# Kernel tuning notes

Measured on AMD Instinct MI355X. Metric: run time of the kernel, lower is better.

## Reference

```python
import jax, jax.numpy as jnp
import numpy as np

TEMPERATURE = 0.1
THRESHOLD = 0.2
EPS = 1e-12


def setup_inputs() -> dict:
    key = jax.random.key(0)
    k0, k1 = jax.random.split(key)
    f0 = jax.random.normal(k0, (1, 256, 80, 80), dtype=jnp.float32)
    f1 = jax.random.normal(k1, (1, 256, 80, 80), dtype=jnp.float32)
    return {"f0": f0, "f1": f1}


def reference(f0, f1):
    B, C, H0, W0 = f0.shape
    _, _, H1, W1 = f1.shape
    N0, N1 = H0 * W0, H1 * W1

    # (B, N, C), L2-normalized along C (matches F.normalize with eps clamp)
    f0_flat = f0.reshape(B, C, N0).transpose(0, 2, 1)
    f1_flat = f1.reshape(B, C, N1).transpose(0, 2, 1)
    f0n = f0_flat / jnp.maximum(jnp.linalg.norm(f0_flat, axis=-1, keepdims=True), EPS)
    f1n = f1_flat / jnp.maximum(jnp.linalg.norm(f1_flat, axis=-1, keepdims=True), EPS)

    # cosine similarity / temperature: (B, N0, N1)
    S = jnp.einsum('bnc,bmc->bnm', f0n, f1n) / TEMPERATURE
    # dual softmax
    P = jax.nn.softmax(S, axis=-1) * jax.nn.softmax(S, axis=-2)

    # mutual nearest-neighbor matching (B == 1 branch)
    conf = jnp.max(P[0], axis=-1)              # (N0,)
    indices0 = jnp.argmax(P[0], axis=-1)       # (N0,) row argmax
    indices1 = jnp.argmax(P[0], axis=-2)       # (N1,) column argmax
    ar0 = jnp.arange(N0)
    mutual = indices1[indices0] == ar0
    valid = mutual & (conf > THRESHOLD)        # (N0,) bool

    # fixed-shape (jit-friendly) match outputs: full grid, zeroed where invalid
    mkpts0 = jnp.stack([ar0 % W0, ar0 // W0], axis=1).astype(jnp.float32)
    mkpts1 = jnp.stack([indices0 % W1, indices0 // W1], axis=1).astype(jnp.float32)
    vf = valid[:, None].astype(jnp.float32)
    mkpts0 = mkpts0 * vf
    mkpts1 = mkpts1 * vf
    mconf = jnp.where(valid, conf, 0.0)

    return (P, mkpts0, mkpts1, mconf, valid)
```

## Files before the change

### kernel.cpp

```cpp
#include <hip/hip_runtime.h>

#define N0 6400
#define NC 256
#define WW 80

using half8   = __attribute__((ext_vector_type(8))) _Float16;
using floatx4 = __attribute__((ext_vector_type(4))) float;
#define GLOBAL_AS __attribute__((address_space(1)))
#define LDS_AS    __attribute__((address_space(3)))

__device__ __forceinline__ unsigned long long packvi(float v, int i) {
    return ((unsigned long long)__float_as_uint(v) << 32) | (unsigned int)i;
}

__global__ __launch_bounds__(256) void knorm(const float* __restrict__ f0,
                                             const float* __restrict__ f1,
                                             float* __restrict__ inv0,
                                             float* __restrict__ inv1) {
    int t = blockIdx.x * 256 + threadIdx.x;
    const float* src = (t < N0) ? f0 : f1;
    int n = (t < N0) ? t : (t - N0);
    float s = 0.f;
#pragma unroll 8
    for (int c = 0; c < NC; ++c) {
        float v = src[c * N0 + n];
        s += v * v;
    }
    float inv = 1.0f / fmaxf(sqrtf(s), 1e-12f);
    if (t < N0) inv0[n] = inv; else inv1[n] = inv;
}

__global__ __launch_bounds__(256) void ktrans(const float* __restrict__ f0,
                                              const float* __restrict__ f1,
                                              const float* __restrict__ inv0,
                                              const float* __restrict__ inv1,
                                              _Float16* __restrict__ A2,
                                              _Float16* __restrict__ B2) {
    __shared__ float tile[32][33];
    const float* src = blockIdx.z ? f1 : f0;
    const float* inv = blockIdx.z ? inv1 : inv0;
    _Float16* dst    = blockIdx.z ? B2 : A2;
    int t = threadIdx.x;
    int n0 = blockIdx.x * 32, c0 = blockIdx.y * 32;
    int tx = t & 31, ty = t >> 5;
#pragma unroll
    for (int u = 0; u < 4; ++u)
        tile[ty + u * 8][tx] = src[(c0 + ty + u * 8) * N0 + n0 + tx];
    __syncthreads();
    int row = t >> 3;
    int cg  = (t & 7) * 4;
    int n = n0 + row;
    float iv = inv[n];
    union { ushort4 u4; _Float16 h[4]; } pk;
#pragma unroll
    for (int u = 0; u < 4; ++u)
        pk.h[u] = (_Float16)(tile[cg + u][row] * iv);
    *(ushort4*)&dst[n * NC + c0 + cg] = pk.u4;
}

__device__ __forceinline__ void stage_panel(const _Float16* __restrict__ G,
                                            unsigned short* lds, int r0, int tid) {
    int rl = tid >> 3;
    int ch = ((tid & 7) ^ (rl & 7)) * 8;
#pragma unroll
    for (int kk = 0; kk < 4; ++kk)
#pragma unroll
        for (int g = 0; g < 4; ++g) {
            const _Float16* ga = G + (r0 + g * 32 + rl) * NC + kk * 64 + ch;
            __builtin_amdgcn_global_load_lds((const GLOBAL_AS unsigned int*)ga,
                (LDS_AS unsigned int*)&lds[kk * 8192 + g * 2048 + tid * 8], 16, 0, 0);
        }
}

__device__ __forceinline__ void tile_mfma(const unsigned short* ldsA,
                                          const unsigned short* ldsB,
                                          int lane, int wm, int wn,
                                          floatx4 acc[4][4]) {
    int q = lane >> 4;
#pragma unroll
    for (int s = 0; s < 8; ++s) {
        int c  = s * 4 + q;
        int kk = c >> 3, cq = c & 7;
        half8 af[4], bf[4];
#pragma unroll
        for (int mt = 0; mt < 4; ++mt) {
            int ra = wm * 64 + mt * 16 + (lane & 15);
            af[mt] = *(const half8*)&ldsA[kk * 8192 + ra * 64 + ((cq ^ (ra & 7)) * 8)];
            int rb = wn * 64 + mt * 16 + (lane & 15);
            bf[mt] = *(const half8*)&ldsB[kk * 8192 + rb * 64 + ((cq ^ (rb & 7)) * 8)];
        }
#pragma unroll
        for (int mt = 0; mt < 4; ++mt)
#pragma unroll
            for (int nt = 0; nt < 4; ++nt)
                acc[mt][nt] = __builtin_amdgcn_mfma_f32_16x16x32_f16(
                    af[mt], bf[nt], acc[mt][nt], 0, 0, 0);
    }
}

__global__ __launch_bounds__(256, 1) void kgemm1(const _Float16* __restrict__ A2,
                                                 const _Float16* __restrict__ B2,
                                                 float* __restrict__ rowsum,
                                                 float* __restrict__ colsum) {
    __shared__ __align__(16) unsigned short ldsA[32768], ldsB[32768];
    int tid = threadIdx.x, lane = tid & 63, wave = tid >> 6;
    int wm = wave & 1, wn = wave >> 1, q = lane >> 4;
    int i0 = blockIdx.x * 128, jp = blockIdx.y * 1280;

    stage_panel(A2, ldsA, i0, tid);
    float rsum[4][4] = {};

    for (int jt = 0; jt < 10; ++jt) {
        __syncthreads();
        stage_panel(B2, ldsB, jp + jt * 128, tid);
        __syncthreads();
        floatx4 acc[4][4] = {};
        tile_mfma(ldsA, ldsB, lane, wm, wn, acc);

        float csum[4] = {0.f, 0.f, 0.f, 0.f};
#pragma unroll
        for (int mt = 0; mt < 4; ++mt)
#pragma unroll
            for (int r = 0; r < 4; ++r) {
                float rv = 0.f;
#pragma unroll
                for (int nt = 0; nt < 4; ++nt) {
                    float e = __expf(10.0f * acc[mt][nt][r]);
                    rv += e; csum[nt] += e;
                }
                rsum[mt][r] += rv;
            }
#pragma unroll
        for (int nt = 0; nt < 4; ++nt) {
            csum[nt] += __shfl_xor(csum[nt], 16);
            csum[nt] += __shfl_xor(csum[nt], 32);
        }
        if (lane < 16)
#pragma unroll
            for (int nt = 0; nt < 4; ++nt)
                atomicAdd(&colsum[jp + jt * 128 + wn * 64 + nt * 16 + lane], csum[nt]);
    }
#pragma unroll
    for (int mt = 0; mt < 4; ++mt)
#pragma unroll
        for (int r = 0; r < 4; ++r) {
            float v = rsum[mt][r];
            v += __shfl_xor(v, 1);
            v += __shfl_xor(v, 2);
            v += __shfl_xor(v, 4);
            v += __shfl_xor(v, 8);
            if ((lane & 15) == 0)
                atomicAdd(&rowsum[i0 + wm * 64 + mt * 16 + q * 4 + r], v);
        }
}

__global__ __launch_bounds__(256, 1) void kgemm2(const _Float16* __restrict__ A2,
                                                 const _Float16* __restrict__ B2,
                                                 const float* __restrict__ rowsum,
                                                 const float* __restrict__ colsum,
                                                 float* __restrict__ P,
                                                 unsigned long long* __restrict__ rowbest,
                                                 unsigned long long* __restrict__ colbest) {
    __shared__ __align__(16) unsigned short ldsA[32768], ldsB[32768];
    int tid = threadIdx.x, lane = tid & 63, wave = tid >> 6;
    int wm = wave & 1, wn = wave >> 1, q = lane >> 4;
    int i0 = blockIdx.x * 128, jp = blockIdx.y * 1280;

    stage_panel(A2, ldsA, i0, tid);

    float ir[4][4];
#pragma unroll
    for (int mt = 0; mt < 4; ++mt) {
        float4 v4 = *(const float4*)&rowsum[i0 + wm * 64 + mt * 16 + q * 4];
        ir[mt][0] = 1.0f / v4.x; ir[mt][1] = 1.0f / v4.y;
        ir[mt][2] = 1.0f / v4.z; ir[mt][3] = 1.0f / v4.w;
    }

    unsigned long long rbv[4][4] = {};

    for (int jt = 0; jt < 10; ++jt) {
        __syncthreads();
        stage_panel(B2, ldsB, jp + jt * 128, tid);
        __syncthreads();
        floatx4 acc[4][4] = {};
        tile_mfma(ldsA, ldsB, lane, wm, wn, acc);

        int cb0 = jp + jt * 128 + wn * 64 + (lane & 15);
        float ic[4];
#pragma unroll
        for (int nt = 0; nt < 4; ++nt) ic[nt] = 1.0f / colsum[cb0 + nt * 16];

        unsigned long long colb[4] = {0ull, 0ull, 0ull, 0ull};
#pragma unroll
        for (int mt = 0; mt < 4; ++mt) {
            int rb0 = i0 + wm * 64 + mt * 16 + q * 4;
#pragma unroll
            for (int r = 0; r < 4; ++r) {
                int row = rb0 + r;
#pragma unroll
                for (int nt = 0; nt < 4; ++nt) {
                    float pv = __expf(20.0f * acc[mt][nt][r]) * ir[mt][r] * ic[nt];
                    P[row * N0 + cb0 + nt * 16] = pv;
                    unsigned long long pr = packvi(pv, cb0 + nt * 16);
                    if (pr > rbv[mt][r]) rbv[mt][r] = pr;
                    unsigned long long pc = packvi(pv, row);
                    if (pc > colb[nt]) colb[nt] = pc;
                }
            }
        }
#pragma unroll
        for (int nt = 0; nt < 4; ++nt) {
            unsigned long long o = __shfl_xor(colb[nt], 16);
            if (o > colb[nt]) colb[nt] = o;
            o = __shfl_xor(colb[nt], 32);
            if (o > colb[nt]) colb[nt] = o;
        }
        if (lane < 16)
#pragma unroll
            for (int nt = 0; nt < 4; ++nt)
                atomicMax(&colbest[cb0 + nt * 16], colb[nt]);
    }
#pragma unroll
    for (int mt = 0; mt < 4; ++mt)
#pragma unroll
        for (int r = 0; r < 4; ++r) {
            unsigned long long v = rbv[mt][r];
#pragma unroll
            for (int s = 1; s < 16; s <<= 1) {
                unsigned long long o = __shfl_xor(v, s);
                if (o > v) v = o;
            }
            if ((lane & 15) == 0)
                atomicMax(&rowbest[i0 + wm * 64 + mt * 16 + q * 4 + r], v);
        }
}

__global__ __launch_bounds__(256) void kmatch(const unsigned long long* __restrict__ rowbest,
                                              const unsigned long long* __restrict__ colbest,
                                              float* __restrict__ out) {
    int i = blockIdx.x * 256 + threadIdx.x;
    unsigned long long rb = rowbest[i];
    float conf = __uint_as_float((unsigned int)(rb >> 32));
    int jj = (int)(rb & 0xffffffffu);
    unsigned long long cb = colbest[jj];
    int i2 = (int)(cb & 0xffffffffu);
    bool valid = (i2 == i) && (conf > 0.2f);
    float vf = valid ? 1.0f : 0.0f;

    float* mk0   = out + 40960000;
    float* mk1   = out + 40972800;
    float* mconf = out + 40985600;
    float* vout  = out + 40992000;
    mk0[i * 2 + 0] = vf * (float)(i % WW);
    mk0[i * 2 + 1] = vf * (float)(i / WW);
    mk1[i * 2 + 0] = vf * (float)(jj % WW);
    mk1[i * 2 + 1] = vf * (float)(jj / WW);
    mconf[i] = valid ? conf : 0.0f;
    vout[i]  = vf;
}

extern "C" void kernel_launch(void* const* d_in, const int* in_sizes, int n_in,
                              void* d_out, int out_size, void* d_ws, size_t ws_size,
                              hipStream_t stream) {
    const float* f0 = (const float*)d_in[0];
    const float* f1 = (const float*)d_in[1];
    float* out = (float*)d_out;

    _Float16* A2 = (_Float16*)d_ws;
    _Float16* B2 = A2 + 6400 * 256;
    float* inv0   = (float*)(B2 + 6400 * 256);
    float* inv1   = inv0 + 6400;
    float* rowsum = inv1 + 6400;
    float* colsum = rowsum + 6400;
    unsigned long long* rowbest = (unsigned long long*)(colsum + 6400);
    unsigned long long* colbest = rowbest + 6400;

    hipMemsetAsync(rowsum, 0, 153600, stream);

    knorm<<<50, 256, 0, stream>>>(f0, f1, inv0, inv1);
    ktrans<<<dim3(200, 8, 2), 256, 0, stream>>>(f0, f1, inv0, inv1, A2, B2);
    kgemm1<<<dim3(50, 5), 256, 0, stream>>>(A2, B2, rowsum, colsum);
    kgemm2<<<dim3(50, 5), 256, 0, stream>>>(A2, B2, rowsum, colsum,
                                            out, rowbest, colbest);
    kmatch<<<25, 256, 0, stream>>>(rowbest, colbest, out);
}
```

Measured before the change: 275.1 us.

## Restructure GEMM kernels with register-resident A, double-buffered B, partial-buffer reductions

The GEMM kernels now use 512 threads with the A panel held in registers, and they double-buffer the B panel in LDS so the next tile loads while the current one computes. Row and column sums and argmax values are written to per-block partial buffers and combined by separate reduce kernels, replacing global atomics and the memset. Argmax comparisons use the log-domain score instead of the exponentiated P, and P is written with vectorized nontemporal stores. The norm kernel is split across two channel halves for more parallelism. Costs are two extra launches and larger workspace traffic. The log-domain argmax risks tie-breaking differences from the reference.

```diff
diff --git a/kernel.cpp b/kernel.cpp
--- a/kernel.cpp
+++ b/kernel.cpp
@@ -15,30 +15,29 @@
 
 __global__ __launch_bounds__(256) void knorm(const float* __restrict__ f0,
                                              const float* __restrict__ f1,
-                                             float* __restrict__ inv0,
-                                             float* __restrict__ inv1) {
-    int t = blockIdx.x * 256 + threadIdx.x;
-    const float* src = (t < N0) ? f0 : f1;
-    int n = (t < N0) ? t : (t - N0);
+                                             float* __restrict__ snorm) {
+    int g = blockIdx.x * 256 + threadIdx.x;
+    int h = (g >= 12800) ? 1 : 0;
+    int j = g - h * 12800;
+    const float* src = (j < N0) ? f0 : f1;
+    int n = (j < N0) ? j : (j - N0);
+    int c0 = h * 128;
     float s = 0.f;
 #pragma unroll 8
-    for (int c = 0; c < NC; ++c) {
-        float v = src[c * N0 + n];
+    for (int c = 0; c < 128; ++c) {
+        float v = src[(c0 + c) * N0 + n];
         s += v * v;
     }
-    float inv = 1.0f / fmaxf(sqrtf(s), 1e-12f);
-    if (t < N0) inv0[n] = inv; else inv1[n] = inv;
+    snorm[g] = s;
 }
 
 __global__ __launch_bounds__(256) void ktrans(const float* __restrict__ f0,
                                               const float* __restrict__ f1,
-                                              const float* __restrict__ inv0,
-                                              const float* __restrict__ inv1,
+                                              const float* __restrict__ snorm,
                                               _Float16* __restrict__ A2,
                                               _Float16* __restrict__ B2) {
     __shared__ float tile[32][33];
     const float* src = blockIdx.z ? f1 : f0;
-    const float* inv = blockIdx.z ? inv1 : inv0;
     _Float16* dst    = blockIdx.z ? B2 : A2;
     int t = threadIdx.x;
     int n0 = blockIdx.x * 32, c0 = blockIdx.y * 32;
@@ -50,7 +49,9 @@
     int row = t >> 3;
     int cg  = (t & 7) * 4;
     int n = n0 + row;
-    float iv = inv[n];
+    int j = (blockIdx.z ? N0 : 0) + n;
+    float s = snorm[j] + snorm[12800 + j];
+    float iv = 1.0f / fmaxf(sqrtf(s), 1e-12f);
     union { ushort4 u4; _Float16 h[4]; } pk;
 #pragma unroll
     for (int u = 0; u < 4; ++u)
@@ -58,192 +59,259 @@
     *(ushort4*)&dst[n * NC + c0 + cg] = pk.u4;
 }
 
-__device__ __forceinline__ void stage_panel(const _Float16* __restrict__ G,
-                                            unsigned short* lds, int r0, int tid) {
+__device__ __forceinline__ void stage_full(const _Float16* __restrict__ G,
+                                           unsigned short* lds, int r0, int tid) {
     int rl = tid >> 3;
     int ch = ((tid & 7) ^ (rl & 7)) * 8;
 #pragma unroll
     for (int kk = 0; kk < 4; ++kk)
 #pragma unroll
-        for (int g = 0; g < 4; ++g) {
-            const _Float16* ga = G + (r0 + g * 32 + rl) * NC + kk * 64 + ch;
+        for (int g = 0; g < 2; ++g) {
+            const _Float16* ga = G + (r0 + g * 64 + rl) * NC + kk * 64 + ch;
             __builtin_amdgcn_global_load_lds((const GLOBAL_AS unsigned int*)ga,
-                (LDS_AS unsigned int*)&lds[kk * 8192 + g * 2048 + tid * 8], 16, 0, 0);
-        }
-}
-
-__device__ __forceinline__ void tile_mfma(const unsigned short* ldsA,
-                                          const unsigned short* ldsB,
-                                          int lane, int wm, int wn,
-                                          floatx4 acc[4][4]) {
+                (LDS_AS unsigned int*)&lds[kk * 8192 + g * 4096 + tid * 8], 16, 0, 0);
+        }
+}
+
+__device__ __forceinline__ void compute_tile(const unsigned short* cur,
+                                             const half8 af[4][8],
+                                             int lane, int wn,
+                                             floatx4 acc[4][2]) {
     int q = lane >> 4;
+    int rb0 = wn * 32 + (lane & 15), rb1 = rb0 + 16;
 #pragma unroll
     for (int s = 0; s < 8; ++s) {
-        int c  = s * 4 + q;
-        int kk = c >> 3, cq = c & 7;
-        half8 af[4], bf[4];
-#pragma unroll
-        for (int mt = 0; mt < 4; ++mt) {
-            int ra = wm * 64 + mt * 16 + (lane & 15);
-            af[mt] = *(const half8*)&ldsA[kk * 8192 + ra * 64 + ((cq ^ (ra & 7)) * 8)];
-            int rb = wn * 64 + mt * 16 + (lane & 15);
-            bf[mt] = *(const half8*)&ldsB[kk * 8192 + rb * 64 + ((cq ^ (rb & 7)) * 8)];
-        }
-#pragma unroll
-        for (int mt = 0; mt < 4; ++mt)
-#pragma unroll
-            for (int nt = 0; nt < 4; ++nt)
-                acc[mt][nt] = __builtin_amdgcn_mfma_f32_16x16x32_f16(
-                    af[mt], bf[nt], acc[mt][nt], 0, 0, 0);
-    }
-}
-
-__global__ __launch_bounds__(256, 1) void kgemm1(const _Float16* __restrict__ A2,
-                                                 const _Float16* __restrict__ B2,
-                                                 float* __restrict__ rowsum,
-                                                 float* __restrict__ colsum) {
-    __shared__ __align__(16) unsigned short ldsA[32768], ldsB[32768];
+        int c = s * 4 + q, kk = c >> 3, cq = c & 7;
+        half8 bf0 = *(const half8*)&cur[kk * 8192 + rb0 * 64 + ((cq ^ (rb0 & 7)) * 8)];
+        half8 bf1 = *(const half8*)&cur[kk * 8192 + rb1 * 64 + ((cq ^ (rb1 & 7)) * 8)];
+#pragma unroll
+        for (int at = 0; at < 4; ++at) {
+            acc[at][0] = __builtin_amdgcn_mfma_f32_16x16x32_f16(bf0, af[at][s], acc[at][0], 0, 0, 0);
+            acc[at][1] = __builtin_amdgcn_mfma_f32_16x16x32_f16(bf1, af[at][s], acc[at][1], 0, 0, 0);
+        }
+    }
+}
+
+__device__ __forceinline__ void gemm_prologue(const _Float16* __restrict__ A2,
+                                              const _Float16* __restrict__ B2,
+                                              unsigned short* lds,
+                                              int i0, int jp, int tid, int lane,
+                                              int wm, half8 af[4][8]) {
+    int q = lane >> 4;
+    stage_full(A2, lds, i0, tid);
+    __syncthreads();
+#pragma unroll
+    for (int at = 0; at < 4; ++at)
+#pragma unroll
+        for (int s = 0; s < 8; ++s) {
+            int c = s * 4 + q, kk = c >> 3, cq = c & 7;
+            int ra = wm * 64 + at * 16 + (lane & 15);
+            af[at][s] = *(const half8*)&lds[kk * 8192 + ra * 64 + ((cq ^ (ra & 7)) * 8)];
+        }
+    stage_full(B2, lds + 32768, jp, tid);
+    __syncthreads();
+}
+
+__global__ __launch_bounds__(512, 2) void kgemm1N(const _Float16* __restrict__ A2,
+                                                  const _Float16* __restrict__ B2,
+                                                  float* __restrict__ rowpart,
+                                                  float* __restrict__ colpart) {
+    __shared__ __align__(16) unsigned short lds[65536];
     int tid = threadIdx.x, lane = tid & 63, wave = tid >> 6;
     int wm = wave & 1, wn = wave >> 1, q = lane >> 4;
     int i0 = blockIdx.x * 128, jp = blockIdx.y * 1280;
 
-    stage_panel(A2, ldsA, i0, tid);
-    float rsum[4][4] = {};
-
+    half8 af[4][8];
+    gemm_prologue(A2, B2, lds, i0, jp, tid, lane, wm, af);
+
+    float rsum[4] = {0.f, 0.f, 0.f, 0.f};
     for (int jt = 0; jt < 10; ++jt) {
+        unsigned short* cur = lds + ((jt & 1) ? 0 : 32768);
+        if (jt < 9)
+            stage_full(B2, lds + ((jt & 1) ? 32768 : 0), jp + (jt + 1) * 128, tid);
+
+        floatx4 acc[4][2] = {};
+        compute_tile(cur, af, lane, wn, acc);
+
+        int jcb = jp + jt * 128;
+        float csum[2][4] = {};
+#pragma unroll
+        for (int at = 0; at < 4; ++at)
+#pragma unroll
+            for (int bt = 0; bt < 2; ++bt)
+#pragma unroll
+                for (int r = 0; r < 4; ++r) {
+                    float e = __expf(10.0f * acc[at][bt][r]);
+                    rsum[at] += e;
+                    csum[bt][r] += e;
+                }
+#pragma unroll
+        for (int bt = 0; bt < 2; ++bt)
+#pragma unroll
+            for (int r = 0; r < 4; ++r) {
+                float v = csum[bt][r];
+                v += __shfl_xor(v, 1);
+                v += __shfl_xor(v, 2);
+                v += __shfl_xor(v, 4);
+                v += __shfl_xor(v, 8);
+                if ((lane & 15) == 0)
+                    colpart[(blockIdx.x * 2 + wm) * N0 + jcb + wn * 32 + bt * 16 + q * 4 + r] = v;
+            }
         __syncthreads();
-        stage_panel(B2, ldsB, jp + jt * 128, tid);
-        __syncthreads();
-        floatx4 acc[4][4] = {};
-        tile_mfma(ldsA, ldsB, lane, wm, wn, acc);
-
-        float csum[4] = {0.f, 0.f, 0.f, 0.f};
-#pragma unroll
-        for (int mt = 0; mt < 4; ++mt)
-#pragma unroll
-            for (int r = 0; r < 4; ++r) {
-                float rv = 0.f;
-#pragma unroll
-                for (int nt = 0; nt < 4; ++nt) {
-                    float e = __expf(10.0f * acc[mt][nt][r]);
-                    rv += e; csum[nt] += e;
-                }
-                rsum[mt][r] += rv;
-            }
-#pragma unroll
-        for (int nt = 0; nt < 4; ++nt) {
-            csum[nt] += __shfl_xor(csum[nt], 16);
-            csum[nt] += __shfl_xor(csum[nt], 32);
-        }
+    }
+#pragma unroll
+    for (int at = 0; at < 4; ++at) {
+        float v = rsum[at];
+        v += __shfl_xor(v, 16);
+        v += __shfl_xor(v, 32);
         if (lane < 16)
-#pragma unroll
-            for (int nt = 0; nt < 4; ++nt)
-                atomicAdd(&colsum[jp + jt * 128 + wn * 64 + nt * 16 + lane], csum[nt]);
-    }
-#pragma unroll
-    for (int mt = 0; mt < 4; ++mt)
-#pragma unroll
-        for (int r = 0; r < 4; ++r) {
-            float v = rsum[mt][r];
-            v += __shfl_xor(v, 1);
-            v += __shfl_xor(v, 2);
-            v += __shfl_xor(v, 4);
-            v += __shfl_xor(v, 8);
-            if ((lane & 15) == 0)
-                atomicAdd(&rowsum[i0 + wm * 64 + mt * 16 + q * 4 + r], v);
-        }
-}
-
-__global__ __launch_bounds__(256, 1) void kgemm2(const _Float16* __restrict__ A2,
-                                                 const _Float16* __restrict__ B2,
-                                                 const float* __restrict__ rowsum,
-                                                 const float* __restrict__ colsum,
-                                                 float* __restrict__ P,
-                                                 unsigned long long* __restrict__ rowbest,
-                                                 unsigned long long* __restrict__ colbest) {
-    __shared__ __align__(16) unsigned short ldsA[32768], ldsB[32768];
+            rowpart[(blockIdx.y * 4 + wn) * N0 + i0 + wm * 64 + at * 16 + lane] = v;
+    }
+}
+
+__global__ __launch_bounds__(256) void kreduce(const float* __restrict__ rowpart,
+                                               const float* __restrict__ colpart,
+                                               float* __restrict__ rowsum,
+                                               float* __restrict__ colsum) {
+    int t = blockIdx.x * 256 + threadIdx.x;
+    if (t < N0) {
+        float s = 0.f;
+#pragma unroll
+        for (int k = 0; k < 20; ++k) s += rowpart[k * N0 + t];
+        rowsum[t] = s;
+    } else {
+        int j = t - N0;
+        float s = 0.f;
+        for (int k = 0; k < 100; ++k) s += colpart[k * N0 + j];
+        colsum[j] = s;
+    }
+}
+
+__global__ __launch_bounds__(512, 2) void kgemm2N(const _Float16* __restrict__ A2,
+                                                  const _Float16* __restrict__ B2,
+                                                  const float* __restrict__ rowsum,
+                                                  const float* __restrict__ colsum,
+                                                  float* __restrict__ P,
+                                                  unsigned long long* __restrict__ rowbpart,
+                                                  unsigned long long* __restrict__ colbpart) {
+    __shared__ __align__(16) unsigned short lds[65536];
     int tid = threadIdx.x, lane = tid & 63, wave = tid >> 6;
     int wm = wave & 1, wn = wave >> 1, q = lane >> 4;
     int i0 = blockIdx.x * 128, jp = blockIdx.y * 1280;
 
-    stage_panel(A2, ldsA, i0, tid);
-
-    float ir[4][4];
-#pragma unroll
-    for (int mt = 0; mt < 4; ++mt) {
-        float4 v4 = *(const float4*)&rowsum[i0 + wm * 64 + mt * 16 + q * 4];
-        ir[mt][0] = 1.0f / v4.x; ir[mt][1] = 1.0f / v4.y;
-        ir[mt][2] = 1.0f / v4.z; ir[mt][3] = 1.0f / v4.w;
-    }
-
-    unsigned long long rbv[4][4] = {};
-
+    half8 af[4][8];
+    gemm_prologue(A2, B2, lds, i0, jp, tid, lane, wm, af);
+
+    float ir[4], lr[4];
+#pragma unroll
+    for (int at = 0; at < 4; ++at) {
+        ir[at] = 1.0f / rowsum[i0 + wm * 64 + at * 16 + (lane & 15)];
+        lr[at] = __logf(ir[at]) * 0.05f + 4.0f;
+    }
+
+    unsigned long long rbv[4] = {};
     for (int jt = 0; jt < 10; ++jt) {
+        unsigned short* cur = lds + ((jt & 1) ? 0 : 32768);
+        if (jt < 9)
+            stage_full(B2, lds + ((jt & 1) ? 32768 : 0), jp + (jt + 1) * 128, tid);
+
+        floatx4 acc[4][2] = {};
+        compute_tile(cur, af, lane, wn, acc);
+
+        int jcb = jp + jt * 128;
+        float ic[2][4], lc[2][4];
+#pragma unroll
+        for (int bt = 0; bt < 2; ++bt) {
+            float4 c4 = *(const float4*)&colsum[jcb + wn * 32 + bt * 16 + q * 4];
+            ic[bt][0] = 1.0f / c4.x; ic[bt][1] = 1.0f / c4.y;
+            ic[bt][2] = 1.0f / c4.z; ic[bt][3] = 1.0f / c4.w;
+#pragma unroll
+            for (int r = 0; r < 4; ++r)
+                lc[bt][r] = __logf(ic[bt][r]) * 0.05f + 4.0f;
+        }
+
+        unsigned long long colb[2][4] = {};
+#pragma unroll
+        for (int at = 0; at < 4; ++at) {
+            int row = i0 + wm * 64 + at * 16 + (lane & 15);
+#pragma unroll
+            for (int bt = 0; bt < 2; ++bt) {
+                floatx4 pv;
+#pragma unroll
+                for (int r = 0; r < 4; ++r) {
+                    float a = acc[at][bt][r];
+                    pv[r] = __expf(20.0f * a) * ir[at] * ic[bt][r];
+                    unsigned long long pr = packvi(a + lc[bt][r],
+                                                   jcb + wn * 32 + bt * 16 + q * 4 + r);
+                    if (pr > rbv[at]) rbv[at] = pr;
+                    unsigned long long pc = packvi(a + lr[at], row);
+                    if (pc > colb[bt][r]) colb[bt][r] = pc;
+                }
+                __builtin_nontemporal_store(pv,
+                    (floatx4*)&P[row * N0 + jcb + wn * 32 + bt * 16 + q * 4]);
+            }
+        }
+#pragma unroll
+        for (int bt = 0; bt < 2; ++bt)
+#pragma unroll
+            for (int r = 0; r < 4; ++r) {
+                unsigned long long v = colb[bt][r];
+#pragma unroll
+                for (int s = 1; s < 16; s <<= 1) {
+                    unsigned long long o = __shfl_xor(v, s);
+                    if (o > v) v = o;
+                }
+                if ((lane & 15) == 0)
+                    colbpart[(blockIdx.x * 2 + wm) * N0 + jcb + wn * 32 + bt * 16 + q * 4 + r] = v;
+            }
         __syncthreads();
-        stage_panel(B2, ldsB, jp + jt * 128, tid);
-        __syncthreads();
-        floatx4 acc[4][4] = {};
-        tile_mfma(ldsA, ldsB, lane, wm, wn, acc);
-
-        int cb0 = jp + jt * 128 + wn * 64 + (lane & 15);
-        float ic[4];
-#pragma unroll
-        for (int nt = 0; nt < 4; ++nt) ic[nt] = 1.0f / colsum[cb0 + nt * 16];
-
-        unsigned long long colb[4] = {0ull, 0ull, 0ull, 0ull};
-#pragma unroll
-        for (int mt = 0; mt < 4; ++mt) {
-            int rb0 = i0 + wm * 64 + mt * 16 + q * 4;
-#pragma unroll
-            for (int r = 0; r < 4; ++r) {
-                int row = rb0 + r;
-#pragma unroll
-                for (int nt = 0; nt < 4; ++nt) {
-                    float pv = __expf(20.0f * acc[mt][nt][r]) * ir[mt][r] * ic[nt];
-                    P[row * N0 + cb0 + nt * 16] = pv;
-                    unsigned long long pr = packvi(pv, cb0 + nt * 16);
-                    if (pr > rbv[mt][r]) rbv[mt][r] = pr;
-                    unsigned long long pc = packvi(pv, row);
-                    if (pc > colb[nt]) colb[nt] = pc;
-                }
-            }
-        }
-#pragma unroll
-        for (int nt = 0; nt < 4; ++nt) {
-            unsigned long long o = __shfl_xor(colb[nt], 16);
-            if (o > colb[nt]) colb[nt] = o;
-            o = __shfl_xor(colb[nt], 32);
-            if (o > colb[nt]) colb[nt] = o;
-        }
+    }
+#pragma unroll
+    for (int at = 0; at < 4; ++at) {
+        unsigned long long v = rbv[at];
+        unsigned long long o = __shfl_xor(v, 16);
+        if (o > v) v = o;
+        o = __shfl_xor(v, 32);
+        if (o > v) v = o;
         if (lane < 16)
-#pragma unroll
-            for (int nt = 0; nt < 4; ++nt)
-                atomicMax(&colbest[cb0 + nt * 16], colb[nt]);
-    }
-#pragma unroll
-    for (int mt = 0; mt < 4; ++mt)
-#pragma unroll
-        for (int r = 0; r < 4; ++r) {
-            unsigned long long v = rbv[mt][r];
-#pragma unroll
-            for (int s = 1; s < 16; s <<= 1) {
-                unsigned long long o = __shfl_xor(v, s);
-                if (o > v) v = o;
-            }
-            if ((lane & 15) == 0)
-                atomicMax(&rowbest[i0 + wm * 64 + mt * 16 + q * 4 + r], v);
-        }
+            rowbpart[(blockIdx.y * 4 + wn) * N0 + i0 + wm * 64 + at * 16 + lane] = v;
+    }
+}
+
+__global__ __launch_bounds__(256) void kreduceB(const unsigned long long* __restrict__ rowbpart,
+                                                const unsigned long long* __restrict__ colbpart,
+                                                unsigned long long* __restrict__ rowbest,
+                                                unsigned long long* __restrict__ colbest) {
+    int t = blockIdx.x * 256 + threadIdx.x;
+    if (t < N0) {
+        unsigned long long m = 0ull;
+#pragma unroll
+        for (int k = 0; k < 20; ++k) {
+            unsigned long long v = rowbpart[k * N0 + t];
+            if (v > m) m = v;
+        }
+        rowbest[t] = m;
+    } else {
+        int j = t - N0;
+        unsigned long long m = 0ull;
+        for (int k = 0; k < 100; ++k) {
+            unsigned long long v = colbpart[k * N0 + j];
+            if (v > m) m = v;
+        }
+        colbest[j] = m;
+    }
 }
 
 __global__ __launch_bounds__(256) void kmatch(const unsigned long long* __restrict__ rowbest,
                                               const unsigned long long* __restrict__ colbest,
+                                              const float* __restrict__ P,
                                               float* __restrict__ out) {
     int i = blockIdx.x * 256 + threadIdx.x;
     unsigned long long rb = rowbest[i];
-    float conf = __uint_as_float((unsigned int)(rb >> 32));
     int jj = (int)(rb & 0xffffffffu);
     unsigned long long cb = colbest[jj];
     int i2 = (int)(cb & 0xffffffffu);
+    float conf = P[i * N0 + jj];
     bool valid = (i2 == i) && (conf > 0.2f);
     float vf = valid ? 1.0f : 0.0f;
 
@@ -268,19 +336,22 @@
 
     _Float16* A2 = (_Float16*)d_ws;
     _Float16* B2 = A2 + 6400 * 256;
-    float* inv0   = (float*)(B2 + 6400 * 256);
-    float* inv1   = inv0 + 6400;
-    float* rowsum = inv1 + 6400;
-    float* colsum = rowsum + 6400;
-    unsigned long long* rowbest = (unsigned long long*)(colsum + 6400);
-    unsigned long long* colbest = rowbest + 6400;
-
-    hipMemsetAsync(rowsum, 0, 153600, stream);
-
-    knorm<<<50, 256, 0, stream>>>(f0, f1, inv0, inv1);
-    ktrans<<<dim3(200, 8, 2), 256, 0, stream>>>(f0, f1, inv0, inv1, A2, B2);
-    kgemm1<<<dim3(50, 5), 256, 0, stream>>>(A2, B2, rowsum, colsum);
-    kgemm2<<<dim3(50, 5), 256, 0, stream>>>(A2, B2, rowsum, colsum,
-                                            out, rowbest, colbest);
-    kmatch<<<25, 256, 0, stream>>>(rowbest, colbest, out);
-}
+    unsigned long long* rowbpart = (unsigned long long*)(B2 + 6400 * 256);
+    unsigned long long* colbpart = rowbpart + 20 * 6400;
+    unsigned long long* rowbest  = colbpart + 100 * 6400;
+    unsigned long long* colbest  = rowbest + 6400;
+    float* snorm   = (float*)(colbest + 6400);
+    float* rowsum  = snorm + 25600;
+    float* colsum  = rowsum + 6400;
+    float* rowpart = colsum + 6400;
+    float* colpart = rowpart + 20 * 6400;
+
+    knorm<<<100, 256, 0, stream>>>(f0, f1, snorm);
+    ktrans<<<dim3(200, 8, 2), 256, 0, stream>>>(f0, f1, snorm, A2, B2);
+    kgemm1N<<<dim3(50, 5), 512, 0, stream>>>(A2, B2, rowpart, colpart);
+    kreduce<<<50, 256, 0, stream>>>(rowpart, colpart, rowsum, colsum);
+    kgemm2N<<<dim3(50, 5), 512, 0, stream>>>(A2, B2, rowsum, colsum,
+                                             out, rowbpart, colbpart);
+    kreduceB<<<50, 256, 0, stream>>>(rowbpart, colbpart, rowbest, colbest);
+    kmatch<<<25, 256, 0, stream>>>(rowbest, colbest, out, out);
+}
```

Measured after the change: 276.8 us. About the same (+0.6%).
